# Performance work log

Measured on AMD Instinct MI355X. Metric: run time of the kernel, lower is better.

The kernel has to match this reference:

```python
import jax, jax.numpy as jnp
import numpy as np

B, C3, H, W = 2, 96, 256, 256   # triplane: 3 planes x 32 channels
CP = C3 // 3                    # per-plane channels = MLP in_channels
VV, S = 128 * 128, 32           # rays, steps per ray
HID, OUT = 64, 33               # hidden, out_feature_channels + 1
NEG_SLOPE = 0.01


def leaky(v):
    return jnp.where(v >= 0, v, NEG_SLOPE * v)


def grid_sample(img, grid):
    """Bilinear grid_sample, align_corners=False, zero padding.
    img: (N, C, H, W); grid: (N, Hg, Wg, 2) with (x, y) in [-1, 1].
    Returns (N, C, Hg, Wg)."""
    N, C, Hi, Wi = img.shape
    x = (grid[..., 0] + 1.0) * (Wi * 0.5) - 0.5
    y = (grid[..., 1] + 1.0) * (Hi * 0.5) - 0.5
    x0 = jnp.floor(x)
    y0 = jnp.floor(y)
    wx = x - x0
    wy = y - y0
    imgf = img.reshape(N, C, Hi * Wi)

    def corner(xi, yi, w):
        valid = (xi >= 0) & (xi < Wi) & (yi >= 0) & (yi < Hi)
        xi_c = jnp.clip(xi, 0, Wi - 1).astype(jnp.int32)
        yi_c = jnp.clip(yi, 0, Hi - 1).astype(jnp.int32)
        idx = yi_c * Wi + xi_c                      # (N, Hg, Wg)
        v = jax.vmap(lambda im, ix: im[:, ix])(imgf, idx)  # (N, C, Hg, Wg)
        return v * (w * valid)[:, None, :, :]

    return (corner(x0, y0, (1 - wx) * (1 - wy))
            + corner(x0 + 1, y0, wx * (1 - wy))
            + corner(x0, y0 + 1, (1 - wx) * wy)
            + corner(x0 + 1, y0 + 1, wx * wy))


def setup_inputs() -> dict:
    key = jax.random.key(0)
    ks = jax.random.split(key, 8)
    triplane = jax.random.normal(ks[0], (B, C3, H, W), jnp.float32)
    # points are normalized coordinates in [-1, 1]
    points = jax.random.uniform(ks[1], (B, VV, S, 3), jnp.float32, -1.0, 1.0)
    W0 = jax.random.normal(ks[2], (CP, HID), jnp.float32) * 0.05
    b0 = jnp.zeros((HID,), jnp.float32)
    W1 = jax.random.normal(ks[3], (HID, HID), jnp.float32) * 0.05
    b1 = jnp.zeros((HID,), jnp.float32)
    W2 = jax.random.normal(ks[4], (HID, OUT), jnp.float32) * 0.05
    b2 = jnp.zeros((OUT,), jnp.float32)
    return {"triplane": triplane, "points": points,
            "W0": W0, "b0": b0, "W1": W1, "b1": b1, "W2": W2, "b2": b2}


def reference(triplane, points, W0, b0, W1, b1, W2, b2):
    Bb = triplane.shape[0]
    xy = points[..., 0:2]
    xz = jnp.stack([points[..., 0], points[..., 2]], axis=-1)
    yz = points[..., 1:3]
    # (B, 3, VV, S, 2) -> (B*3, VV, S, 2)
    grid = jnp.stack([xy, xz, yz], axis=1).reshape(Bb * 3, *xy.shape[1:])
    planes = triplane.reshape(Bb * 3, -1, triplane.shape[-2], triplane.shape[-1])
    feat = grid_sample(planes, grid)                      # (B*3, CP, VV, S)
    feat = feat.reshape(Bb, 3, -1, feat.shape[-2], feat.shape[-1]).sum(axis=1)
    feat = feat.transpose(0, 2, 3, 1)                     # (B, VV, S, CP)
    h = leaky(feat @ W0 + b0)
    h = leaky(h @ W1 + b1)
    return h @ W2 + b2                                    # (B, VV, S, OUT)
```

## Files before the change

### kernel.cpp

```cpp
#include <hip/hip_runtime.h>

#define BATCH 2
#define PLANES 3
#define CP 32
#define HH 256
#define WW 256
#define HWSZ 65536
#define HID 64
#define NOUT 33
#define NPTS_TOTAL 1048576
#define PLANE_ELEMS 2097152
#define PLANE_ELEMS_DUP 4194304
#define MPTS 128

typedef unsigned int u32;
typedef unsigned short u16;
typedef float floatx4 __attribute__((ext_vector_type(4)));
typedef short bf16x8 __attribute__((ext_vector_type(8)));

static __device__ __forceinline__ u16 f2bf(float f) {
    u32 u = __float_as_uint(f);
    return (u16)((u + 0x7fffu + ((u >> 16) & 1u)) >> 16);
}
static __device__ __forceinline__ float bflo(u32 u) { return __uint_as_float(u << 16); }
static __device__ __forceinline__ float bfhi(u32 u) { return __uint_as_float(u & 0xffff0000u); }

__global__ __launch_bounds__(256) void transpose_dup_k(const float* __restrict__ tp,
                                                       u16* __restrict__ out) {
    int idx = blockIdx.x * 256 + threadIdx.x;
    int bp = idx >> 16;
    int yx = idx & 65535;
    int x = yx & 255;
    int b = bp / 3, p = bp - 3 * b;
    const float* src = tp + (((size_t)(b * 96 + p * 32)) << 16) + yx;
    const bool hasx1 = (x < 255);
    u16 v0[32], v1[32];
#pragma unroll
    for (int c = 0; c < 32; ++c) {
        v0[c] = f2bf(src[(size_t)c << 16]);
        v1[c] = hasx1 ? f2bf(src[((size_t)c << 16) + 1]) : (u16)0;
    }
    uint4* dst = (uint4*)(out + ((size_t)idx << 6));
#pragma unroll
    for (int i = 0; i < 8; ++i) {
        uint4 w;
        w.x = (u32)v0[4 * i + 0] | ((u32)v1[4 * i + 0] << 16);
        w.y = (u32)v0[4 * i + 1] | ((u32)v1[4 * i + 1] << 16);
        w.z = (u32)v0[4 * i + 2] | ((u32)v1[4 * i + 2] << 16);
        w.w = (u32)v0[4 * i + 3] | ((u32)v1[4 * i + 3] << 16);
        dst[i] = w;
    }
}

__global__ __launch_bounds__(256, 2) void fused_mfma_k(const u16* __restrict__ planes,
                                                       const float* __restrict__ points,
                                                       const float* __restrict__ W0,
                                                       const float* __restrict__ b0,
                                                       const float* __restrict__ W1,
                                                       const float* __restrict__ b1,
                                                       const float* __restrict__ W2,
                                                       const float* __restrict__ b2,
                                                       float* __restrict__ out) {
    __shared__ __align__(16) u16 sW0t[64 * 40];
    __shared__ __align__(16) u16 sW1t[64 * 72];
    __shared__ __align__(16) u16 sW2t[48 * 72];
    __shared__ __align__(16) u16 sR0[MPTS * 72];
    __shared__ __align__(16) u16 sR1[MPTS * 72];
    __shared__ float sB0[64], sB1[64], sB2[33];

    const int tid = threadIdx.x;
    for (int i = tid; i < 32 * 64; i += 256) { int k = i >> 6, m = i & 63; sW0t[m * 40 + k] = f2bf(W0[i]); }
    for (int i = tid; i < 64 * 64; i += 256) { int k = i >> 6, m = i & 63; sW1t[m * 72 + k] = f2bf(W1[i]); }
    for (int i = tid; i < 64 * 33; i += 256) { int k = i / 33, m = i - 33 * k; sW2t[m * 72 + k] = f2bf(W2[i]); }
    if (tid < 64) { sB0[tid] = b0[tid]; sB1[tid] = b1[tid]; }
    if (tid < 33) sB2[tid] = b2[tid];

    const size_t pbase = (size_t)blockIdx.x * MPTS;
    float* sPts = (float*)sR1;
    for (int i = tid; i < MPTS * 3; i += 256) sPts[i] = points[pbase * 3 + i];
    __syncthreads();

    const int bBatch = blockIdx.x >> 12;
#pragma unroll
    for (int t = 0; t < 2; ++t) {
        const int task = t * 256 + tid;
        const int pt = task >> 2, q = task & 3;
        const float px = sPts[pt * 3 + 0];
        const float py = sPts[pt * 3 + 1];
        const float pz = sPts[pt * 3 + 2];
        float acc[8];
#pragma unroll
        for (int j = 0; j < 8; ++j) acc[j] = 0.f;
#pragma unroll
        for (int p = 0; p < PLANES; ++p) {
            const float gx = (p == 2) ? py : px;
            const float gy = (p == 0) ? py : pz;
            const float x = (gx + 1.0f) * 128.0f - 0.5f;
            const float y = (gy + 1.0f) * 128.0f - 0.5f;
            const float xf = floorf(x), yf = floorf(y);
            const float wx = x - xf, wy = y - yf;
            const int ix0 = (int)xf, iy0 = (int)yf;
            const int xb = max(ix0, 0);
            const float ax = (ix0 >= 0) ? (1.f - wx) : wx;
            const float bx = (ix0 >= 0) ? wx : 0.f;
            const u16* pb = planes + ((size_t)(bBatch * 3 + p) << 22);
#pragma unroll
            for (int r = 0; r < 2; ++r) {
                const int iy = iy0 + r;
                const bool vy = (iy >= 0) & (iy < HH);
                const float wrow = (r ? wy : (1.f - wy));
                const float wa = vy ? wrow * ax : 0.f;
                const float wb = vy ? wrow * bx : 0.f;
                const int iyc = min(max(iy, 0), HH - 1);
                const u16* src = pb + (((size_t)((iyc << 8) | xb)) << 6) + (q << 4);
                const uint4 d0 = *(const uint4*)src;
                const uint4 d1 = *(const uint4*)(src + 8);
#pragma unroll
                for (int j = 0; j < 4; ++j) {
                    const u32 u = (&d0.x)[j];
                    acc[j] = fmaf(wa, bflo(u), fmaf(wb, bfhi(u), acc[j]));
                    const u32 u2 = (&d1.x)[j];
                    acc[4 + j] = fmaf(wa, bflo(u2), fmaf(wb, bfhi(u2), acc[4 + j]));
                }
            }
        }
        uint4 o;
        o.x = (u32)f2bf(acc[0]) | ((u32)f2bf(acc[1]) << 16);
        o.y = (u32)f2bf(acc[2]) | ((u32)f2bf(acc[3]) << 16);
        o.z = (u32)f2bf(acc[4]) | ((u32)f2bf(acc[5]) << 16);
        o.w = (u32)f2bf(acc[6]) | ((u32)f2bf(acc[7]) << 16);
        *(uint4*)(sR0 + pt * 40 + q * 8) = o;
    }
    __syncthreads();

    const int lane = tid & 63, wv = tid >> 6;
    const int ln = lane & 15, qd = lane >> 4;

    bf16x8 a0[4];
#pragma unroll
    for (int mt = 0; mt < 4; ++mt)
        a0[mt] = *(const bf16x8*)(sW0t + (mt * 16 + ln) * 40 + qd * 8);
    bf16x8 bx0[2];
#pragma unroll
    for (int nt = 0; nt < 2; ++nt)
        bx0[nt] = *(const bf16x8*)(sR0 + (wv * 32 + nt * 16 + ln) * 40 + qd * 8);
    floatx4 acc0[2][4];
#pragma unroll
    for (int nt = 0; nt < 2; ++nt)
#pragma unroll
        for (int mt = 0; mt < 4; ++mt) {
            floatx4 z = {0.f, 0.f, 0.f, 0.f};
            acc0[nt][mt] = __builtin_amdgcn_mfma_f32_16x16x32_bf16(a0[mt], bx0[nt], z, 0, 0, 0);
        }
#pragma unroll
    for (int nt = 0; nt < 2; ++nt) {
        const int n = wv * 32 + nt * 16 + ln;
#pragma unroll
        for (int mt = 0; mt < 4; ++mt) {
            u16 p[4];
#pragma unroll
            for (int r = 0; r < 4; ++r) {
                const int m = mt * 16 + qd * 4 + r;
                float v = acc0[nt][mt][r] + sB0[m];
                v = (v >= 0.f) ? v : 0.01f * v;
                p[r] = f2bf(v);
            }
            uint2 dd = make_uint2((u32)p[0] | ((u32)p[1] << 16), (u32)p[2] | ((u32)p[3] << 16));
            *(uint2*)(sR1 + n * 72 + mt * 16 + qd * 4) = dd;
        }
    }

    bf16x8 a1[4][2];
#pragma unroll
    for (int mt = 0; mt < 4; ++mt)
#pragma unroll
        for (int c = 0; c < 2; ++c)
            a1[mt][c] = *(const bf16x8*)(sW1t + (mt * 16 + ln) * 72 + c * 32 + qd * 8);
    floatx4 acc1[2][4];
#pragma unroll
    for (int nt = 0; nt < 2; ++nt) {
        const int n = wv * 32 + nt * 16 + ln;
        bf16x8 bf0 = *(const bf16x8*)(sR1 + n * 72 + qd * 8);
        bf16x8 bf1 = *(const bf16x8*)(sR1 + n * 72 + 32 + qd * 8);
#pragma unroll
        for (int mt = 0; mt < 4; ++mt) {
            floatx4 z = {0.f, 0.f, 0.f, 0.f};
            floatx4 t = __builtin_amdgcn_mfma_f32_16x16x32_bf16(a1[mt][0], bf0, z, 0, 0, 0);
            acc1[nt][mt] = __builtin_amdgcn_mfma_f32_16x16x32_bf16(a1[mt][1], bf1, t, 0, 0, 0);
        }
    }
    __syncthreads();

#pragma unroll
    for (int nt = 0; nt < 2; ++nt) {
        const int n = wv * 32 + nt * 16 + ln;
#pragma unroll
        for (int mt = 0; mt < 4; ++mt) {
            u16 p[4];
#pragma unroll
            for (int r = 0; r < 4; ++r) {
                const int m = mt * 16 + qd * 4 + r;
                float v = acc1[nt][mt][r] + sB1[m];
                v = (v >= 0.f) ? v : 0.01f * v;
                p[r] = f2bf(v);
            }
            uint2 dd = make_uint2((u32)p[0] | ((u32)p[1] << 16), (u32)p[2] | ((u32)p[3] << 16));
            *(uint2*)(sR0 + n * 72 + mt * 16 + qd * 4) = dd;
        }
    }

    bf16x8 a2[3][2];
#pragma unroll
    for (int mt = 0; mt < 3; ++mt)
#pragma unroll
        for (int c = 0; c < 2; ++c)
            a2[mt][c] = *(const bf16x8*)(sW2t + (mt * 16 + ln) * 72 + c * 32 + qd * 8);
    floatx4 acc2[2][3];
#pragma unroll
    for (int nt = 0; nt < 2; ++nt) {
        const int n = wv * 32 + nt * 16 + ln;
        bf16x8 bf0 = *(const bf16x8*)(sR0 + n * 72 + qd * 8);
        bf16x8 bf1 = *(const bf16x8*)(sR0 + n * 72 + 32 + qd * 8);
#pragma unroll
        for (int mt = 0; mt < 3; ++mt) {
            floatx4 z = {0.f, 0.f, 0.f, 0.f};
            floatx4 t = __builtin_amdgcn_mfma_f32_16x16x32_bf16(a2[mt][0], bf0, z, 0, 0, 0);
            acc2[nt][mt] = __builtin_amdgcn_mfma_f32_16x16x32_bf16(a2[mt][1], bf1, t, 0, 0, 0);
        }
    }
    __syncthreads();

    float* sOut = (float*)sR1;
#pragma unroll
    for (int nt = 0; nt < 2; ++nt) {
        const int n = wv * 32 + nt * 16 + ln;
#pragma unroll
        for (int mt = 0; mt < 3; ++mt)
#pragma unroll
            for (int r = 0; r < 4; ++r) {
                const int m = mt * 16 + qd * 4 + r;
                if (m < NOUT) sOut[n * 36 + m] = acc2[nt][mt][r] + sB2[m];
            }
    }
    __syncthreads();

    float* og = out + pbase * NOUT;
    for (int i = tid; i < MPTS * NOUT; i += 256) {
        int n = i / 33, m = i - 33 * n;
        og[i] = sOut[n * 36 + m];
    }
}

__global__ __launch_bounds__(256) void transpose_bf16_k(const float* __restrict__ tp,
                                                        u16* __restrict__ out) {
    int idx = blockIdx.x * 256 + threadIdx.x;
    int bp = idx >> 16;
    int yx = idx & 65535;
    int b = bp / 3, p = bp - 3 * b;
    const float* src = tp + (((size_t)(b * 96 + p * 32)) << 16) + yx;
    u16 v[32];
#pragma unroll
    for (int c = 0; c < 32; ++c) v[c] = f2bf(src[(size_t)c << 16]);
    uint4* dst = (uint4*)(out + ((size_t)idx << 5));
#pragma unroll
    for (int i = 0; i < 4; ++i) {
        uint4 w;
        w.x = (u32)v[8 * i + 0] | ((u32)v[8 * i + 1] << 16);
        w.y = (u32)v[8 * i + 2] | ((u32)v[8 * i + 3] << 16);
        w.z = (u32)v[8 * i + 4] | ((u32)v[8 * i + 5] << 16);
        w.w = (u32)v[8 * i + 6] | ((u32)v[8 * i + 7] << 16);
        dst[i] = w;
    }
}

__global__ __launch_bounds__(256) void fused2_k(const u16* __restrict__ planes,
                                                const float* __restrict__ points,
                                                const float* __restrict__ W0,
                                                const float* __restrict__ b0,
                                                const float* __restrict__ W1,
                                                const float* __restrict__ b1,
                                                const float* __restrict__ W2,
                                                const float* __restrict__ b2,
                                                float* __restrict__ out) {
    __shared__ __align__(16) float sPts[256 * 3];
    __shared__ __align__(16) float sFeat[256 * 33];
    const int tid = threadIdx.x;
    const int blockBase = blockIdx.x * 256;
    const int b = blockIdx.x >> 11;
    const float* psrc = points + (size_t)blockBase * 3;
#pragma unroll
    for (int i = 0; i < 3; ++i) sPts[tid + 256 * i] = psrc[tid + 256 * i];
    __syncthreads();
#pragma unroll
    for (int i = 0; i < 4; ++i) {
        const int task = i * 256 + tid;
        const int pt = task >> 2, q = task & 3;
        const float px = sPts[pt * 3 + 0], py = sPts[pt * 3 + 1], pz = sPts[pt * 3 + 2];
        float acc[8];
#pragma unroll
        for (int j = 0; j < 8; ++j) acc[j] = 0.f;
#pragma unroll
        for (int p = 0; p < PLANES; ++p) {
            const float gx = (p == 2) ? py : px;
            const float gy = (p == 0) ? py : pz;
            const float x = (gx + 1.0f) * 128.0f - 0.5f;
            const float y = (gy + 1.0f) * 128.0f - 0.5f;
            const float xf = floorf(x), yf = floorf(y);
            const float wx = x - xf, wy = y - yf;
            const int ix0 = (int)xf, iy0 = (int)yf;
            const u16* pb = planes + (size_t)(b * 3 + p) * PLANE_ELEMS + q * 8;
            auto corner = [&](int ix, int iy, float w) {
                const bool v = (ix >= 0) & (ix < WW) & (iy >= 0) & (iy < HH);
                w = v ? w : 0.f;
                const int ixc = min(max(ix, 0), WW - 1);
                const int iyc = min(max(iy, 0), HH - 1);
                const int yx = (iyc << 8) | ixc;
                const uint4 d = *(const uint4*)(pb + ((size_t)yx << 5));
#pragma unroll
                for (int j = 0; j < 4; ++j) {
                    const u32 u = (&d.x)[j];
                    acc[2 * j + 0] = fmaf(w, __uint_as_float(u << 16), acc[2 * j + 0]);
                    acc[2 * j + 1] = fmaf(w, __uint_as_float(u & 0xffff0000u), acc[2 * j + 1]);
                }
            };
            corner(ix0,     iy0,     (1.f - wx) * (1.f - wy));
            corner(ix0 + 1, iy0,     wx * (1.f - wy));
            corner(ix0,     iy0 + 1, (1.f - wx) * wy);
            corner(ix0 + 1, iy0 + 1, wx * wy);
        }
        float* dst = sFeat + pt * 33 + q * 8;
#pragma unroll
        for (int j = 0; j < 8; ++j) dst[j] = acc[j];
    }
    __syncthreads();
    float feat[CP];
#pragma unroll
    for (int c = 0; c < CP; ++c) feat[c] = sFeat[tid * 33 + c];
    float h0[HID];
#pragma unroll
    for (int j = 0; j < HID; ++j) h0[j] = b0[j];
    for (int k = 0; k < CP; ++k) {
        const float f = feat[k];
        const float4* row = (const float4*)(W0 + k * HID);
#pragma unroll
        for (int j4 = 0; j4 < HID / 4; ++j4) {
            const float4 w = row[j4];
            h0[4 * j4 + 0] = fmaf(f, w.x, h0[4 * j4 + 0]);
            h0[4 * j4 + 1] = fmaf(f, w.y, h0[4 * j4 + 1]);
            h0[4 * j4 + 2] = fmaf(f, w.z, h0[4 * j4 + 2]);
            h0[4 * j4 + 3] = fmaf(f, w.w, h0[4 * j4 + 3]);
        }
    }
#pragma unroll
    for (int j = 0; j < HID; ++j) h0[j] = (h0[j] >= 0.f) ? h0[j] : 0.01f * h0[j];
    float h1[HID];
#pragma unroll
    for (int j = 0; j < HID; ++j) h1[j] = b1[j];
    for (int k = 0; k < HID; ++k) {
        const float f = h0[k];
        const float4* row = (const float4*)(W1 + k * HID);
#pragma unroll
        for (int j4 = 0; j4 < HID / 4; ++j4) {
            const float4 w = row[j4];
            h1[4 * j4 + 0] = fmaf(f, w.x, h1[4 * j4 + 0]);
            h1[4 * j4 + 1] = fmaf(f, w.y, h1[4 * j4 + 1]);
            h1[4 * j4 + 2] = fmaf(f, w.z, h1[4 * j4 + 2]);
            h1[4 * j4 + 3] = fmaf(f, w.w, h1[4 * j4 + 3]);
        }
    }
#pragma unroll
    for (int j = 0; j < HID; ++j) h1[j] = (h1[j] >= 0.f) ? h1[j] : 0.01f * h1[j];
    float o[NOUT];
#pragma unroll
    for (int j = 0; j < NOUT; ++j) o[j] = b2[j];
    for (int k = 0; k < HID; ++k) {
        const float f = h1[k];
        const float* row = W2 + k * NOUT;
#pragma unroll
        for (int j = 0; j < NOUT; ++j) o[j] = fmaf(f, row[j], o[j]);
    }
#pragma unroll
    for (int j = 0; j < NOUT; ++j) sFeat[tid * 33 + j] = o[j];
    __syncthreads();
    float4* dst4 = (float4*)(out + (size_t)blockBase * NOUT);
    const float4* src4 = (const float4*)sFeat;
    for (int v = tid; v < (256 * NOUT) / 4; v += 256) dst4[v] = src4[v];
}

__global__ __launch_bounds__(256) void fused_fallback_k(const float* __restrict__ planes,
                                                        const float* __restrict__ points,
                                                        const float* __restrict__ W0,
                                                        const float* __restrict__ b0,
                                                        const float* __restrict__ W1,
                                                        const float* __restrict__ b1,
                                                        const float* __restrict__ W2,
                                                        const float* __restrict__ b2,
                                                        float* __restrict__ out) {
    const int tid = threadIdx.x;
    const int pgl = blockIdx.x * 256 + tid;
    const int b = pgl >> 19;
    const float px = points[(size_t)pgl * 3 + 0];
    const float py = points[(size_t)pgl * 3 + 1];
    const float pz = points[(size_t)pgl * 3 + 2];
    float feat[CP];
#pragma unroll
    for (int c = 0; c < CP; ++c) feat[c] = 0.f;
#pragma unroll
    for (int p = 0; p < PLANES; ++p) {
        const float gx = (p == 2) ? py : px;
        const float gy = (p == 0) ? py : pz;
        const float x = (gx + 1.0f) * 128.0f - 0.5f;
        const float y = (gy + 1.0f) * 128.0f - 0.5f;
        const float xf = floorf(x), yf = floorf(y);
        const float wx = x - xf, wy = y - yf;
        const int ix0 = (int)xf, iy0 = (int)yf;
        const float* pb = planes + (((size_t)(b * 96 + p * 32)) << 16);
        auto corner = [&](int ix, int iy, float w) {
            const bool v = (ix >= 0) & (ix < WW) & (iy >= 0) & (iy < HH);
            w = v ? w : 0.f;
            const int ixc = min(max(ix, 0), WW - 1);
            const int iyc = min(max(iy, 0), HH - 1);
            const int yx = (iyc << 8) | ixc;
            const float* src = pb + yx;
#pragma unroll
            for (int c = 0; c < CP; ++c) feat[c] = fmaf(w, src[(size_t)c << 16], feat[c]);
        };
        corner(ix0,     iy0,     (1.f - wx) * (1.f - wy));
        corner(ix0 + 1, iy0,     wx * (1.f - wy));
        corner(ix0,     iy0 + 1, (1.f - wx) * wy);
        corner(ix0 + 1, iy0 + 1, wx * wy);
    }
    float h0[HID];
#pragma unroll
    for (int j = 0; j < HID; ++j) h0[j] = b0[j];
    for (int k = 0; k < CP; ++k) {
        const float f = feat[k];
#pragma unroll
        for (int j = 0; j < HID; ++j) h0[j] = fmaf(f, W0[k * HID + j], h0[j]);
    }
#pragma unroll
    for (int j = 0; j < HID; ++j) h0[j] = (h0[j] >= 0.f) ? h0[j] : 0.01f * h0[j];
    float h1[HID];
#pragma unroll
    for (int j = 0; j < HID; ++j) h1[j] = b1[j];
    for (int k = 0; k < HID; ++k) {
        const float f = h0[k];
#pragma unroll
        for (int j = 0; j < HID; ++j) h1[j] = fmaf(f, W1[k * HID + j], h1[j]);
    }
#pragma unroll
    for (int j = 0; j < HID; ++j) h1[j] = (h1[j] >= 0.f) ? h1[j] : 0.01f * h1[j];
    float o[NOUT];
#pragma unroll
    for (int j = 0; j < NOUT; ++j) o[j] = b2[j];
    for (int k = 0; k < HID; ++k) {
        const float f = h1[k];
#pragma unroll
        for (int j = 0; j < NOUT; ++j) o[j] = fmaf(f, W2[k * NOUT + j], o[j]);
    }
    float* op = out + (size_t)pgl * NOUT;
#pragma unroll
    for (int j = 0; j < NOUT; ++j) op[j] = o[j];
}

extern "C" void kernel_launch(void* const* d_in, const int* in_sizes, int n_in,
                              void* d_out, int out_size, void* d_ws, size_t ws_size,
                              hipStream_t stream) {
    const float* triplane = (const float*)d_in[0];
    const float* points   = (const float*)d_in[1];
    const float* W0 = (const float*)d_in[2];
    const float* b0 = (const float*)d_in[3];
    const float* W1 = (const float*)d_in[4];
    const float* b1 = (const float*)d_in[5];
    const float* W2 = (const float*)d_in[6];
    const float* b2 = (const float*)d_in[7];
    float* out = (float*)d_out;

    const size_t needDup    = (size_t)BATCH * PLANES * PLANE_ELEMS_DUP * sizeof(u16);
    const size_t needPlanes = (size_t)BATCH * PLANES * PLANE_ELEMS * sizeof(u16);

    if (d_ws != nullptr && ws_size >= needDup) {
        u16* planesW = (u16*)d_ws;
        transpose_dup_k<<<(BATCH * PLANES * HWSZ) / 256, 256, 0, stream>>>(triplane, planesW);
        fused_mfma_k<<<NPTS_TOTAL / MPTS, 256, 0, stream>>>(planesW, points, W0, b0, W1, b1, W2, b2, out);
    } else if (d_ws != nullptr && ws_size >= needPlanes) {
        u16* planesW = (u16*)d_ws;
        transpose_bf16_k<<<(BATCH * PLANES * HWSZ) / 256, 256, 0, stream>>>(triplane, planesW);
        fused2_k<<<NPTS_TOTAL / 256, 256, 0, stream>>>(planesW, points, W0, b0, W1, b1, W2, b2, out);
    } else {
        fused_fallback_k<<<NPTS_TOTAL / 256, 256, 0, stream>>>(
            triplane, points, W0, b0, W1, b1, W2, b2, out);
    }
}
```

Measured before the change: 393.2 us.

## Split fused gather+MLP into separate gather and MFMA MLP kernels

Replaces the single fused sampling+MLP kernel with two kernels. A gather kernel uses 8 threads per point to bilinearly sample the duplicated-x bf16 planes and writes bf16 features to workspace. A separate MFMA MLP kernel then reads those features. Splitting is meant to let the latency-bound gather run at higher occupancy, apart from the MLP's shared-memory footprint. The cost is an extra round trip of roughly 64 MB of features through global memory, and it needs more workspace. The old non-dup fused2 path is removed.

```diff
diff --git a/kernel.cpp b/kernel.cpp
--- a/kernel.cpp
+++ b/kernel.cpp
@@ -49,6 +49,205 @@
         w.z = (u32)v0[4 * i + 2] | ((u32)v1[4 * i + 2] << 16);
         w.w = (u32)v0[4 * i + 3] | ((u32)v1[4 * i + 3] << 16);
         dst[i] = w;
+    }
+}
+
+__global__ __launch_bounds__(256) void gather_dup_k(const u16* __restrict__ planes,
+                                                    const float* __restrict__ points,
+                                                    u16* __restrict__ feats) {
+    const int task = blockIdx.x * 256 + threadIdx.x;
+    const int pt = task >> 3;
+    const int o = task & 7;
+    const int b = pt >> 19;
+    const float px = points[(size_t)pt * 3 + 0];
+    const float py = points[(size_t)pt * 3 + 1];
+    const float pz = points[(size_t)pt * 3 + 2];
+
+    float acc[4];
+#pragma unroll
+    for (int j = 0; j < 4; ++j) acc[j] = 0.f;
+
+#pragma unroll
+    for (int p = 0; p < PLANES; ++p) {
+        const float gx = (p == 2) ? py : px;
+        const float gy = (p == 0) ? py : pz;
+        const float x = (gx + 1.0f) * 128.0f - 0.5f;
+        const float y = (gy + 1.0f) * 128.0f - 0.5f;
+        const float xf = floorf(x), yf = floorf(y);
+        const float wx = x - xf, wy = y - yf;
+        const int ix0 = (int)xf, iy0 = (int)yf;
+        const int xb = max(ix0, 0);
+        const float ax = (ix0 >= 0) ? (1.f - wx) : wx;
+        const float bx = (ix0 >= 0) ? wx : 0.f;
+        const u16* pb = planes + ((size_t)(b * 3 + p) << 22);
+#pragma unroll
+        for (int r = 0; r < 2; ++r) {
+            const int iy = iy0 + r;
+            const bool vy = (iy >= 0) & (iy < HH);
+            const float wrow = (r ? wy : (1.f - wy));
+            const float wa = vy ? wrow * ax : 0.f;
+            const float wb = vy ? wrow * bx : 0.f;
+            const int iyc = min(max(iy, 0), HH - 1);
+            const uint4 d = *(const uint4*)(pb + (((size_t)((iyc << 8) | xb)) << 6) + (o << 3));
+#pragma unroll
+            for (int j = 0; j < 4; ++j) {
+                const u32 u = (&d.x)[j];
+                acc[j] = fmaf(wa, bflo(u), fmaf(wb, bfhi(u), acc[j]));
+            }
+        }
+    }
+
+    uint2 w;
+    w.x = (u32)f2bf(acc[0]) | ((u32)f2bf(acc[1]) << 16);
+    w.y = (u32)f2bf(acc[2]) | ((u32)f2bf(acc[3]) << 16);
+    *(uint2*)(feats + (size_t)pt * 32 + o * 4) = w;
+}
+
+__global__ __launch_bounds__(256) void mlp_k(const u16* __restrict__ feats,
+                                             const float* __restrict__ W0,
+                                             const float* __restrict__ b0,
+                                             const float* __restrict__ W1,
+                                             const float* __restrict__ b1,
+                                             const float* __restrict__ W2,
+                                             const float* __restrict__ b2,
+                                             float* __restrict__ out) {
+    __shared__ __align__(16) u16 sW0t[64 * 40];
+    __shared__ __align__(16) u16 sW1t[64 * 72];
+    __shared__ __align__(16) u16 sW2t[48 * 72];
+    __shared__ __align__(16) u16 sR0[MPTS * 72];
+    __shared__ __align__(16) u16 sR1[MPTS * 72];
+    __shared__ float sB0[64], sB1[64], sB2[33];
+
+    const int tid = threadIdx.x;
+    for (int i = tid; i < 32 * 64; i += 256) { int k = i >> 6, m = i & 63; sW0t[m * 40 + k] = f2bf(W0[i]); }
+    for (int i = tid; i < 64 * 64; i += 256) { int k = i >> 6, m = i & 63; sW1t[m * 72 + k] = f2bf(W1[i]); }
+    for (int i = tid; i < 64 * 33; i += 256) { int k = i / 33, m = i - 33 * k; sW2t[m * 72 + k] = f2bf(W2[i]); }
+    if (tid < 64) { sB0[tid] = b0[tid]; sB1[tid] = b1[tid]; }
+    if (tid < 33) sB2[tid] = b2[tid];
+
+    const size_t pbase = (size_t)blockIdx.x * MPTS;
+    for (int i = tid; i < MPTS * 4; i += 256) {
+        int pt = i >> 2, q = i & 3;
+        uint4 d = *(const uint4*)(feats + (pbase + pt) * 32 + q * 8);
+        *(uint4*)(sR0 + pt * 40 + q * 8) = d;
+    }
+    __syncthreads();
+
+    const int lane = tid & 63, wv = tid >> 6;
+    const int ln = lane & 15, qd = lane >> 4;
+
+    bf16x8 a0[4];
+#pragma unroll
+    for (int mt = 0; mt < 4; ++mt)
+        a0[mt] = *(const bf16x8*)(sW0t + (mt * 16 + ln) * 40 + qd * 8);
+    bf16x8 bx0[2];
+#pragma unroll
+    for (int nt = 0; nt < 2; ++nt)
+        bx0[nt] = *(const bf16x8*)(sR0 + (wv * 32 + nt * 16 + ln) * 40 + qd * 8);
+    floatx4 acc0[2][4];
+#pragma unroll
+    for (int nt = 0; nt < 2; ++nt)
+#pragma unroll
+        for (int mt = 0; mt < 4; ++mt) {
+            floatx4 z = {0.f, 0.f, 0.f, 0.f};
+            acc0[nt][mt] = __builtin_amdgcn_mfma_f32_16x16x32_bf16(a0[mt], bx0[nt], z, 0, 0, 0);
+        }
+#pragma unroll
+    for (int nt = 0; nt < 2; ++nt) {
+        const int n = wv * 32 + nt * 16 + ln;
+#pragma unroll
+        for (int mt = 0; mt < 4; ++mt) {
+            u16 p[4];
+#pragma unroll
+            for (int r = 0; r < 4; ++r) {
+                const int m = mt * 16 + qd * 4 + r;
+                float v = acc0[nt][mt][r] + sB0[m];
+                v = (v >= 0.f) ? v : 0.01f * v;
+                p[r] = f2bf(v);
+            }
+            uint2 dd = make_uint2((u32)p[0] | ((u32)p[1] << 16), (u32)p[2] | ((u32)p[3] << 16));
+            *(uint2*)(sR1 + n * 72 + mt * 16 + qd * 4) = dd;
+        }
+    }
+
+    bf16x8 a1[4][2];
+#pragma unroll
+    for (int mt = 0; mt < 4; ++mt)
+#pragma unroll
+        for (int c = 0; c < 2; ++c)
+            a1[mt][c] = *(const bf16x8*)(sW1t + (mt * 16 + ln) * 72 + c * 32 + qd * 8);
+    floatx4 acc1[2][4];
+#pragma unroll
+    for (int nt = 0; nt < 2; ++nt) {
+        const int n = wv * 32 + nt * 16 + ln;
+        bf16x8 bf0 = *(const bf16x8*)(sR1 + n * 72 + qd * 8);
+        bf16x8 bf1 = *(const bf16x8*)(sR1 + n * 72 + 32 + qd * 8);
+#pragma unroll
+        for (int mt = 0; mt < 4; ++mt) {
+            floatx4 z = {0.f, 0.f, 0.f, 0.f};
+            floatx4 t = __builtin_amdgcn_mfma_f32_16x16x32_bf16(a1[mt][0], bf0, z, 0, 0, 0);
+            acc1[nt][mt] = __builtin_amdgcn_mfma_f32_16x16x32_bf16(a1[mt][1], bf1, t, 0, 0, 0);
+        }
+    }
+    __syncthreads();
+
+#pragma unroll
+    for (int nt = 0; nt < 2; ++nt) {
+        const int n = wv * 32 + nt * 16 + ln;
+#pragma unroll
+        for (int mt = 0; mt < 4; ++mt) {
+            u16 p[4];
+#pragma unroll
+            for (int r = 0; r < 4; ++r) {
+                const int m = mt * 16 + qd * 4 + r;
+                float v = acc1[nt][mt][r] + sB1[m];
+                v = (v >= 0.f) ? v : 0.01f * v;
+                p[r] = f2bf(v);
+            }
+            uint2 dd = make_uint2((u32)p[0] | ((u32)p[1] << 16), (u32)p[2] | ((u32)p[3] << 16));
+            *(uint2*)(sR0 + n * 72 + mt * 16 + qd * 4) = dd;
+        }
+    }
+
+    bf16x8 a2[3][2];
+#pragma unroll
+    for (int mt = 0; mt < 3; ++mt)
+#pragma unroll
+        for (int c = 0; c < 2; ++c)
+            a2[mt][c] = *(const bf16x8*)(sW2t + (mt * 16 + ln) * 72 + c * 32 + qd * 8);
+    floatx4 acc2[2][3];
+#pragma unroll
+    for (int nt = 0; nt < 2; ++nt) {
+        const int n = wv * 32 + nt * 16 + ln;
+        bf16x8 bf0 = *(const bf16x8*)(sR0 + n * 72 + qd * 8);
+        bf16x8 bf1 = *(const bf16x8*)(sR0 + n * 72 + 32 + qd * 8);
+#pragma unroll
+        for (int mt = 0; mt < 3; ++mt) {
+            floatx4 z = {0.f, 0.f, 0.f, 0.f};
+            floatx4 t = __builtin_amdgcn_mfma_f32_16x16x32_bf16(a2[mt][0], bf0, z, 0, 0, 0);
+            acc2[nt][mt] = __builtin_amdgcn_mfma_f32_16x16x32_bf16(a2[mt][1], bf1, t, 0, 0, 0);
+        }
+    }
+    __syncthreads();
+
+    float* sOut = (float*)sR1;
+#pragma unroll
+    for (int nt = 0; nt < 2; ++nt) {
+        const int n = wv * 32 + nt * 16 + ln;
+#pragma unroll
+        for (int mt = 0; mt < 3; ++mt)
+#pragma unroll
+            for (int r = 0; r < 4; ++r) {
+                const int m = mt * 16 + qd * 4 + r;
+                if (m < NOUT) sOut[n * 36 + m] = acc2[nt][mt][r] + sB2[m];
+            }
+    }
+    __syncthreads();
+
+    float* og = out + pbase * NOUT;
+    for (int i = tid; i < MPTS * NOUT; i += 256) {
+        int n = i / 33, m = i - 33 * n;
+        og[i] = sOut[n * 36 + m];
     }
 }
 
@@ -249,142 +448,6 @@
         int n = i / 33, m = i - 33 * n;
         og[i] = sOut[n * 36 + m];
     }
-}
-
-__global__ __launch_bounds__(256) void transpose_bf16_k(const float* __restrict__ tp,
-                                                        u16* __restrict__ out) {
-    int idx = blockIdx.x * 256 + threadIdx.x;
-    int bp = idx >> 16;
-    int yx = idx & 65535;
-    int b = bp / 3, p = bp - 3 * b;
-    const float* src = tp + (((size_t)(b * 96 + p * 32)) << 16) + yx;
-    u16 v[32];
-#pragma unroll
-    for (int c = 0; c < 32; ++c) v[c] = f2bf(src[(size_t)c << 16]);
-    uint4* dst = (uint4*)(out + ((size_t)idx << 5));
-#pragma unroll
-    for (int i = 0; i < 4; ++i) {
-        uint4 w;
-        w.x = (u32)v[8 * i + 0] | ((u32)v[8 * i + 1] << 16);
-        w.y = (u32)v[8 * i + 2] | ((u32)v[8 * i + 3] << 16);
-        w.z = (u32)v[8 * i + 4] | ((u32)v[8 * i + 5] << 16);
-        w.w = (u32)v[8 * i + 6] | ((u32)v[8 * i + 7] << 16);
-        dst[i] = w;
-    }
-}
-
-__global__ __launch_bounds__(256) void fused2_k(const u16* __restrict__ planes,
-                                                const float* __restrict__ points,
-                                                const float* __restrict__ W0,
-                                                const float* __restrict__ b0,
-                                                const float* __restrict__ W1,
-                                                const float* __restrict__ b1,
-                                                const float* __restrict__ W2,
-                                                const float* __restrict__ b2,
-                                                float* __restrict__ out) {
-    __shared__ __align__(16) float sPts[256 * 3];
-    __shared__ __align__(16) float sFeat[256 * 33];
-    const int tid = threadIdx.x;
-    const int blockBase = blockIdx.x * 256;
-    const int b = blockIdx.x >> 11;
-    const float* psrc = points + (size_t)blockBase * 3;
-#pragma unroll
-    for (int i = 0; i < 3; ++i) sPts[tid + 256 * i] = psrc[tid + 256 * i];
-    __syncthreads();
-#pragma unroll
-    for (int i = 0; i < 4; ++i) {
-        const int task = i * 256 + tid;
-        const int pt = task >> 2, q = task & 3;
-        const float px = sPts[pt * 3 + 0], py = sPts[pt * 3 + 1], pz = sPts[pt * 3 + 2];
-        float acc[8];
-#pragma unroll
-        for (int j = 0; j < 8; ++j) acc[j] = 0.f;
-#pragma unroll
-        for (int p = 0; p < PLANES; ++p) {
-            const float gx = (p == 2) ? py : px;
-            const float gy = (p == 0) ? py : pz;
-            const float x = (gx + 1.0f) * 128.0f - 0.5f;
-            const float y = (gy + 1.0f) * 128.0f - 0.5f;
-            const float xf = floorf(x), yf = floorf(y);
-            const float wx = x - xf, wy = y - yf;
-            const int ix0 = (int)xf, iy0 = (int)yf;
-            const u16* pb = planes + (size_t)(b * 3 + p) * PLANE_ELEMS + q * 8;
-            auto corner = [&](int ix, int iy, float w) {
-                const bool v = (ix >= 0) & (ix < WW) & (iy >= 0) & (iy < HH);
-                w = v ? w : 0.f;
-                const int ixc = min(max(ix, 0), WW - 1);
-                const int iyc = min(max(iy, 0), HH - 1);
-                const int yx = (iyc << 8) | ixc;
-                const uint4 d = *(const uint4*)(pb + ((size_t)yx << 5));
-#pragma unroll
-                for (int j = 0; j < 4; ++j) {
-                    const u32 u = (&d.x)[j];
-                    acc[2 * j + 0] = fmaf(w, __uint_as_float(u << 16), acc[2 * j + 0]);
-                    acc[2 * j + 1] = fmaf(w, __uint_as_float(u & 0xffff0000u), acc[2 * j + 1]);
-                }
-            };
-            corner(ix0,     iy0,     (1.f - wx) * (1.f - wy));
-            corner(ix0 + 1, iy0,     wx * (1.f - wy));
-            corner(ix0,     iy0 + 1, (1.f - wx) * wy);
-            corner(ix0 + 1, iy0 + 1, wx * wy);
-        }
-        float* dst = sFeat + pt * 33 + q * 8;
-#pragma unroll
-        for (int j = 0; j < 8; ++j) dst[j] = acc[j];
-    }
-    __syncthreads();
-    float feat[CP];
-#pragma unroll
-    for (int c = 0; c < CP; ++c) feat[c] = sFeat[tid * 33 + c];
-    float h0[HID];
-#pragma unroll
-    for (int j = 0; j < HID; ++j) h0[j] = b0[j];
-    for (int k = 0; k < CP; ++k) {
-        const float f = feat[k];
-        const float4* row = (const float4*)(W0 + k * HID);
-#pragma unroll
-        for (int j4 = 0; j4 < HID / 4; ++j4) {
-            const float4 w = row[j4];
-            h0[4 * j4 + 0] = fmaf(f, w.x, h0[4 * j4 + 0]);
-            h0[4 * j4 + 1] = fmaf(f, w.y, h0[4 * j4 + 1]);
-            h0[4 * j4 + 2] = fmaf(f, w.z, h0[4 * j4 + 2]);
-            h0[4 * j4 + 3] = fmaf(f, w.w, h0[4 * j4 + 3]);
-        }
-    }
-#pragma unroll
-    for (int j = 0; j < HID; ++j) h0[j] = (h0[j] >= 0.f) ? h0[j] : 0.01f * h0[j];
-    float h1[HID];
-#pragma unroll
-    for (int j = 0; j < HID; ++j) h1[j] = b1[j];
-    for (int k = 0; k < HID; ++k) {
-        const float f = h0[k];
-        const float4* row = (const float4*)(W1 + k * HID);
-#pragma unroll
-        for (int j4 = 0; j4 < HID / 4; ++j4) {
-            const float4 w = row[j4];
-            h1[4 * j4 + 0] = fmaf(f, w.x, h1[4 * j4 + 0]);
-            h1[4 * j4 + 1] = fmaf(f, w.y, h1[4 * j4 + 1]);
-            h1[4 * j4 + 2] = fmaf(f, w.z, h1[4 * j4 + 2]);
-            h1[4 * j4 + 3] = fmaf(f, w.w, h1[4 * j4 + 3]);
-        }
-    }
-#pragma unroll
-    for (int j = 0; j < HID; ++j) h1[j] = (h1[j] >= 0.f) ? h1[j] : 0.01f * h1[j];
-    float o[NOUT];
-#pragma unroll
-    for (int j = 0; j < NOUT; ++j) o[j] = b2[j];
-    for (int k = 0; k < HID; ++k) {
-        const float f = h1[k];
-        const float* row = W2 + k * NOUT;
-#pragma unroll
-        for (int j = 0; j < NOUT; ++j) o[j] = fmaf(f, row[j], o[j]);
-    }
-#pragma unroll
-    for (int j = 0; j < NOUT; ++j) sFeat[tid * 33 + j] = o[j];
-    __syncthreads();
-    float4* dst4 = (float4*)(out + (size_t)blockBase * NOUT);
-    const float4* src4 = (const float4*)sFeat;
-    for (int v = tid; v < (256 * NOUT) / 4; v += 256) dst4[v] = src4[v];
 }
 
 __global__ __launch_bounds__(256) void fused_fallback_k(const float* __restrict__ planes,
@@ -476,17 +539,19 @@
     const float* b2 = (const float*)d_in[7];
     float* out = (float*)d_out;
 
-    const size_t needDup    = (size_t)BATCH * PLANES * PLANE_ELEMS_DUP * sizeof(u16);
-    const size_t needPlanes = (size_t)BATCH * PLANES * PLANE_ELEMS * sizeof(u16);
-
-    if (d_ws != nullptr && ws_size >= needDup) {
+    const size_t needDup   = (size_t)BATCH * PLANES * PLANE_ELEMS_DUP * sizeof(u16);
+    const size_t needFeats = (size_t)NPTS_TOTAL * 32 * sizeof(u16);
+
+    if (d_ws != nullptr && ws_size >= needDup + needFeats) {
+        u16* planesW = (u16*)d_ws;
+        u16* featsW  = planesW + (size_t)BATCH * PLANES * PLANE_ELEMS_DUP;
+        transpose_dup_k<<<(BATCH * PLANES * HWSZ) / 256, 256, 0, stream>>>(triplane, planesW);
+        gather_dup_k<<<(NPTS_TOTAL * 8) / 256, 256, 0, stream>>>(planesW, points, featsW);
+        mlp_k<<<NPTS_TOTAL / MPTS, 256, 0, stream>>>(featsW, W0, b0, W1, b1, W2, b2, out);
+    } else if (d_ws != nullptr && ws_size >= needDup) {
         u16* planesW = (u16*)d_ws;
         transpose_dup_k<<<(BATCH * PLANES * HWSZ) / 256, 256, 0, stream>>>(triplane, planesW);
         fused_mfma_k<<<NPTS_TOTAL / MPTS, 256, 0, stream>>>(planesW, points, W0, b0, W1, b1, W2, b2, out);
-    } else if (d_ws != nullptr && ws_size >= needPlanes) {
-        u16* planesW = (u16*)d_ws;
-        transpose_bf16_k<<<(BATCH * PLANES * HWSZ) / 256, 256, 0, stream>>>(triplane, planesW);
-        fused2_k<<<NPTS_TOTAL / 256, 256, 0, stream>>>(planesW, points, W0, b0, W1, b1, W2, b2, out);
     } else {
         fused_fallback_k<<<NPTS_TOTAL / 256, 256, 0, stream>>>(
             triplane, points, W0, b0, W1, b1, W2, b2, out);
```

New measurement: 417.8 us. +6.2%, slower.
